# Kernel tuning notes

Measured on AMD Instinct MI355X. Metric: run time of the kernel, lower is better.

Reference implementation:

```python
import jax, jax.numpy as jnp
import numpy as np

DIM = 1024
HEADS = 16
DHEAD = 64
INNER = HEADS * DHEAD
EPS = 1e-5


def layer_norm(x, g, b):
    mu = jnp.mean(x, axis=-1, keepdims=True)
    var = jnp.mean(jnp.square(x - mu), axis=-1, keepdims=True)
    return (x - mu) * jax.lax.rsqrt(var + EPS) * g + b


def apply_rope(x, cos, sin):
    # x: [b, h, s, d]; cos/sin broadcast as [1, 1, s, d/2]
    d2 = x.shape[-1] // 2
    x1, x2 = x[..., :d2], x[..., d2:]
    return jnp.concatenate([x1 * cos - x2 * sin, x2 * cos + x1 * sin], axis=-1)


def setup_inputs() -> dict:
    key = jax.random.key(0)
    ks = jax.random.split(key, 10)
    B, N, S = 8, 256, 4096
    latents = jax.random.normal(ks[0], (B, N, DIM), dtype=jnp.float32)
    context = jax.random.normal(ks[1], (B, S, DIM), dtype=jnp.float32)
    cos = jax.random.uniform(ks[2], (S, DHEAD // 2), dtype=jnp.float32)
    sin = jax.random.uniform(ks[3], (S, DHEAD // 2), dtype=jnp.float32)
    init = lambda k, shp, fan_in: jax.random.normal(k, shp, dtype=jnp.float32) / np.sqrt(fan_in)
    return {
        "latents": latents,
        "context": context,
        "cos": cos,
        "sin": sin,
        "ln_lat_g": jnp.ones((DIM,), jnp.float32),
        "ln_lat_b": jnp.zeros((DIM,), jnp.float32),
        "ln_ctx_g": jnp.ones((DIM,), jnp.float32),
        "ln_ctx_b": jnp.zeros((DIM,), jnp.float32),
        "Wq": init(ks[4], (DIM, INNER), DIM),
        "Wkv": init(ks[5], (DIM, 2 * INNER), DIM),
        "Wo": init(ks[6], (INNER, DIM), INNER),
        "bo": jnp.zeros((DIM,), jnp.float32),
    }


def reference(latents, context, cos, sin, ln_lat_g, ln_lat_b, ln_ctx_g, ln_ctx_b, Wq, Wkv, Wo, bo):
    b, n, _ = latents.shape
    s = context.shape[1]
    lat = layer_norm(latents, ln_lat_g, ln_lat_b)
    ctx = layer_norm(context, ln_ctx_g, ln_ctx_b)
    q = (lat @ Wq).reshape(b, n, HEADS, DHEAD).transpose(0, 2, 1, 3)   # [b,h,n,d]
    kv = ctx @ Wkv
    k, v = jnp.split(kv, 2, axis=-1)
    k = k.reshape(b, s, HEADS, DHEAD).transpose(0, 2, 1, 3)           # [b,h,s,d]
    v = v.reshape(b, s, HEADS, DHEAD).transpose(0, 2, 1, 3)
    k = apply_rope(k, cos[None, None], sin[None, None])
    scale = DHEAD ** (-0.5)
    attn = jnp.einsum('bhnd,bhsd->bhns', q, k) * scale
    attn = jnp.clip(attn, -11.0, 11.0)
    attn = jax.nn.softmax(attn, axis=-1)
    out = jnp.einsum('bhns,bhsd->bhnd', attn, v)
    out = out.transpose(0, 2, 1, 3).reshape(b, n, INNER)
    return out @ Wo + bo
```

## Files before the change

kernel.cpp:

```cpp
#include <hip/hip_runtime.h>
#include <hip/hip_bf16.h>
#include <math.h>

#define DIM   1024
#define HEADS 16
#define DHEAD 64
#define NB    8
#define NLAT  256
#define SCTX  4096

typedef short bf16x8 __attribute__((ext_vector_type(8)));
typedef float f32x4  __attribute__((ext_vector_type(4)));

__device__ __forceinline__ unsigned short f2b(float f) {
    union { float f; unsigned u; } x; x.f = f;
    unsigned r = x.u + 0x7FFFu + ((x.u >> 16) & 1u);
    return (unsigned short)(r >> 16);
}

__device__ __forceinline__ unsigned pkbf16(float a, float b) {
    float2 f2; f2.x = a; f2.y = b;
    __hip_bfloat162 h = __float22bfloat162_rn(f2);
    union { __hip_bfloat162 h; unsigned u; } cv; cv.h = h;
    return cv.u;
}

#define LN_BLOCKS (NB * NLAT + NB * SCTX)
__global__ __launch_bounds__(256) void prep_all(
    const float* __restrict__ latents, const float* __restrict__ context,
    const float* __restrict__ g_lat, const float* __restrict__ b_lat,
    const float* __restrict__ g_ctx, const float* __restrict__ b_ctx,
    const float* __restrict__ Wq, const float* __restrict__ Wkv,
    const float* __restrict__ Wo,
    unsigned short* __restrict__ lat_b, unsigned short* __restrict__ ctx_b,
    unsigned short* __restrict__ Wqb, unsigned short* __restrict__ Wkvb,
    unsigned short* __restrict__ Wob)
{
    __shared__ unsigned short tile[32][33];
    int gb = blockIdx.x, t = threadIdx.x;
    if (gb < LN_BLOCKS) {
        const float* x; const float* g; const float* b; unsigned short* y; int r;
        if (gb < NB * NLAT) { x = latents; g = g_lat; b = b_lat; y = lat_b; r = gb; }
        else { x = context; g = g_ctx; b = b_ctx; y = ctx_b; r = gb - NB * NLAT; }
        float* ls = (float*)tile;
        float* lq = ls + 4;
        float* st = ls + 8;
        float4 v = ((const float4*)(x + (size_t)r * DIM))[t];
        float s  = v.x + v.y + v.z + v.w;
        float sq = v.x * v.x + v.y * v.y + v.z * v.z + v.w * v.w;
        #pragma unroll
        for (int off = 32; off > 0; off >>= 1) {
            s  += __shfl_down(s, off);
            sq += __shfl_down(sq, off);
        }
        int wid = t >> 6, lane = t & 63;
        if (lane == 0) { ls[wid] = s; lq[wid] = sq; }
        __syncthreads();
        if (t == 0) {
            s  = ls[0] + ls[1] + ls[2] + ls[3];
            sq = lq[0] + lq[1] + lq[2] + lq[3];
            float m   = s * (1.0f / DIM);
            float var = sq * (1.0f / DIM) - m * m;
            st[0] = m;
            st[1] = rsqrtf(var + 1e-5f);
        }
        __syncthreads();
        float mu = st[0], rs = st[1];
        float4 gg = ((const float4*)g)[t];
        float4 bb = ((const float4*)b)[t];
        ushort4 o;
        o.x = f2b((v.x - mu) * rs * gg.x + bb.x);
        o.y = f2b((v.y - mu) * rs * gg.y + bb.y);
        o.z = f2b((v.z - mu) * rs * gg.z + bb.z);
        o.w = f2b((v.w - mu) * rs * gg.w + bb.w);
        ((ushort4*)(y + (size_t)r * DIM))[t] = o;
    } else {
        int id = gb - LN_BLOCKS;
        int z = id >> 10, y = (id >> 5) & 31, xb = id & 31;
        const float* W; unsigned short* Wt; int N, coloff = 0;
        switch (z) {
            case 0: W = Wq;  Wt = Wqb;  N = DIM;     break;
            case 1: W = Wkv; Wt = Wkvb; N = 2 * DIM; break;
            case 2: W = Wkv; Wt = Wkvb; N = 2 * DIM; coloff = DIM; break;
            default: W = Wo; Wt = Wob;  N = DIM;     break;
        }
        int n0 = xb * 32 + coloff, k0 = y * 32;
        int tx = t & 31, ty = t >> 5;
        #pragma unroll
        for (int i = 0; i < 4; ++i) {
            int k = k0 + ty + i * 8;
            tile[tx][ty + i * 8] = f2b(W[(size_t)k * N + n0 + tx]);
        }
        __syncthreads();
        #pragma unroll
        for (int i = 0; i < 4; ++i) {
            int n = n0 + ty + i * 8;
            Wt[(size_t)n * DIM + k0 + tx] = tile[ty + i * 8][tx];
        }
    }
}

#define GK 1024

#define MFMA_Q(i0, j0)                                                         \
    _Pragma("unroll")                                                          \
    for (int ii = 0; ii < 4; ++ii) {                                           \
        _Pragma("unroll")                                                      \
        for (int jj = 0; jj < 2; ++jj) {                                       \
            acc[(i0) + ii][(j0) + jj] = __builtin_amdgcn_mfma_f32_16x16x32_bf16( \
                a[ii][0], b[(j0) + jj][0], acc[(i0) + ii][(j0) + jj], 0, 0, 0);  \
            acc[(i0) + ii][(j0) + jj] = __builtin_amdgcn_mfma_f32_16x16x32_bf16( \
                a[ii][1], b[(j0) + jj][1], acc[(i0) + ii][(j0) + jj], 0, 0, 0);  \
        }                                                                      \
    }

__global__ __launch_bounds__(512, 2) void gemm256(
    const unsigned short* __restrict__ Akv, const unsigned short* __restrict__ Bkv,
    const unsigned short* __restrict__ Aq,  const unsigned short* __restrict__ Bq,
    const float* __restrict__ cosp, const float* __restrict__ sinp,
    unsigned short* __restrict__ outk, unsigned short* __restrict__ outv,
    unsigned short* __restrict__ outq)
{
    __shared__ __align__(16) unsigned short As[2][16384];
    __shared__ __align__(16) unsigned short Bs[2][16384];

    int t = threadIdx.x;
    int w = t >> 6, l = t & 63;
    int wr = w >> 2, wc = w & 3;
    int quad = l >> 4, ln = l & 15;

    int g = blockIdx.x;
    const unsigned short* A; const unsigned short* B;
    int m_tile, n_tile, isq;
    if (g < 1024) {
        int xcd = g & 7, j = g >> 3;
        n_tile = j & 7;
        m_tile = xcd * 16 + (j >> 3);
        A = Akv; B = Bkv; isq = 0;
    } else {
        g -= 1024;
        n_tile = g & 3;
        m_tile = g >> 2;
        A = Aq; B = Bq; isq = 1;
    }
    int m_base = m_tile * 256, n_base = n_tile * 256;
    const unsigned short* Ag = A + (size_t)m_base * GK;
    const unsigned short* Bg = B + (size_t)n_base * GK;

    f32x4 acc[8][4];
    {
        f32x4 zero = {0.f, 0.f, 0.f, 0.f};
        #pragma unroll
        for (int i = 0; i < 8; ++i)
            #pragma unroll
            for (int j = 0; j < 4; ++j) acc[i][j] = zero;
    }

    int srow = l >> 3;
    int schk = ((l & 7) ^ srow) * 8;

    auto STAGE = [&](const unsigned short* src, int k0, unsigned short* dst) {
        #pragma unroll
        for (int jj = 0; jj < 2; ++jj) {
            int row = jj * 64 + w * 8 + srow;
            __builtin_amdgcn_global_load_lds(
                (const __attribute__((address_space(1))) void*)(src + (size_t)row * GK + k0 + schk),
                (__attribute__((address_space(3))) void*)(dst + row * 64 + (l & 7) * 8),
                16, 0, 0);
        }
    };

    STAGE(Ag,                     0, As[0]);
    STAGE(Ag + 128 * (size_t)GK,  0, As[0] + 8192);
    STAGE(Bg,                     0, Bs[0]);
    STAGE(Bg + 128 * (size_t)GK,  0, Bs[0] + 8192);
    STAGE(Bg,                    64, Bs[1]);
    STAGE(Bg + 128 * (size_t)GK, 64, Bs[1] + 8192);
    asm volatile("s_waitcnt vmcnt(4)" ::: "memory");
    __builtin_amdgcn_s_barrier();

    for (int kt = 0; kt < 16; ++kt) {
        int buf = kt & 1;
        const unsigned short* Ab = As[buf] + wr * 8192;
        const unsigned short* Bb = Bs[buf] + (wc >> 1) * 8192;
        int bloc = (wc & 1) * 64;
        int xs = ln & 7;
        bf16x8 a[4][2], b[4][2];

        #pragma unroll
        for (int i = 0; i < 4; ++i)
            #pragma unroll
            for (int kk = 0; kk < 2; ++kk)
                a[i][kk] = *(const bf16x8*)(Ab + (i * 16 + ln) * 64 + (((kk * 4 + quad) ^ xs) << 3));
        #pragma unroll
        for (int j = 0; j < 2; ++j)
            #pragma unroll
            for (int kk = 0; kk < 2; ++kk)
                b[j][kk] = *(const bf16x8*)(Bb + (bloc + j * 16 + ln) * 64 + (((kk * 4 + quad) ^ xs) << 3));
        if (kt + 1 < 16) {
            int k0 = (kt + 1) * 64;
            STAGE(Ag,                    k0, As[buf ^ 1]);
            STAGE(Ag + 128 * (size_t)GK, k0, As[buf ^ 1] + 8192);
        }
        __builtin_amdgcn_s_barrier();
        asm volatile("s_waitcnt lgkmcnt(0)" ::: "memory");
        __builtin_amdgcn_sched_barrier(0);
        __builtin_amdgcn_s_setprio(1);
        MFMA_Q(0, 0)
        __builtin_amdgcn_s_setprio(0);
        __builtin_amdgcn_s_barrier();

        #pragma unroll
        for (int j = 0; j < 2; ++j)
            #pragma unroll
            for (int kk = 0; kk < 2; ++kk)
                b[2 + j][kk] = *(const bf16x8*)(Bb + (bloc + (2 + j) * 16 + ln) * 64 + (((kk * 4 + quad) ^ xs) << 3));
        __builtin_amdgcn_s_barrier();
        asm volatile("s_waitcnt lgkmcnt(0)" ::: "memory");
        __builtin_amdgcn_sched_barrier(0);
        __builtin_amdgcn_s_setprio(1);
        MFMA_Q(0, 2)
        __builtin_amdgcn_s_setprio(0);
        __builtin_amdgcn_s_barrier();

        #pragma unroll
        for (int i = 0; i < 4; ++i)
            #pragma unroll
            for (int kk = 0; kk < 2; ++kk)
                a[i][kk] = *(const bf16x8*)(Ab + ((4 + i) * 16 + ln) * 64 + (((kk * 4 + quad) ^ xs) << 3));
        if (kt + 2 < 16) STAGE(Bg, (kt + 2) * 64, Bs[buf]);
        __builtin_amdgcn_s_barrier();
        asm volatile("s_waitcnt lgkmcnt(0)" ::: "memory");
        __builtin_amdgcn_sched_barrier(0);
        __builtin_amdgcn_s_setprio(1);
        MFMA_Q(4, 2)
        __builtin_amdgcn_s_setprio(0);
        __builtin_amdgcn_s_barrier();

        if (kt + 2 < 16) STAGE(Bg + 128 * (size_t)GK, (kt + 2) * 64, Bs[buf] + 8192);
        __builtin_amdgcn_s_barrier();
        __builtin_amdgcn_s_setprio(1);
        MFMA_Q(4, 0)
        __builtin_amdgcn_s_setprio(0);
        if (kt + 2 < 16) asm volatile("s_waitcnt vmcnt(4)" ::: "memory");
        else             asm volatile("s_waitcnt vmcnt(0)" ::: "memory");
        __builtin_amdgcn_s_barrier();
    }

    if (!isq) {
        if (n_base >= DIM) {
            #pragma unroll
            for (int i = 0; i < 8; ++i) {
                int s0 = m_base + wr * 128 + i * 16 + quad * 4;
                int bb = s0 >> 12, s = s0 & 4095;
                #pragma unroll
                for (int j = 0; j < 4; ++j) {
                    int n2 = n_base + wc * 64 + j * 16 + ln - DIM;
                    int h = n2 >> 6, d = n2 & 63;
                    ushort4 pk;
                    pk.x = f2b(acc[i][j][0]); pk.y = f2b(acc[i][j][1]);
                    pk.z = f2b(acc[i][j][2]); pk.w = f2b(acc[i][j][3]);
                    *(ushort4*)(outv + (((size_t)(bb * HEADS + h) * DHEAD + d) * SCTX) + s) = pk;
                }
            }
        } else {
            #pragma unroll
            for (int i = 0; i < 8; ++i) {
                #pragma unroll
                for (int r = 0; r < 4; ++r) {
                    int m = m_base + wr * 128 + i * 16 + quad * 4 + r;
                    int bb = m >> 12, s = m & 4095;
                    #pragma unroll
                    for (int j = 0; j < 2; ++j) {
                        int n = n_base + wc * 64 + j * 16 + ln;
                        int h = n >> 6, d1 = n & 63;
                        float x1 = acc[i][j][r], x2 = acc[i][j + 2][r];
                        float c  = cosp[s * 32 + d1];
                        float sn = sinp[s * 32 + d1];
                        unsigned short* kr =
                            outk + (((size_t)(bb * HEADS + h) * SCTX + s) * DHEAD) + d1;
                        kr[0]  = f2b(x1 * c - x2 * sn);
                        kr[32] = f2b(x2 * c + x1 * sn);
                    }
                }
            }
        }
    } else {
        #pragma unroll
        for (int i = 0; i < 8; ++i)
            #pragma unroll
            for (int j = 0; j < 4; ++j)
                #pragma unroll
                for (int r = 0; r < 4; ++r) {
                    int m = m_base + wr * 128 + i * 16 + quad * 4 + r;
                    int n = n_base + wc * 64 + j * 16 + ln;
                    int bb = m >> 8, nn = m & 255;
                    int h = n >> 6, d = n & 63;
                    outq[(((size_t)(bb * HEADS + h) * NLAT + nn) * DHEAD) + d] =
                        f2b(acc[i][j][r] * 0.125f);
                }
    }
}

__global__ __launch_bounds__(256, 2) void gemm_mfma(
    const unsigned short* __restrict__ A, const unsigned short* __restrict__ Bn,
    const unsigned short* __restrict__ Aq, const unsigned short* __restrict__ Bq,
    int K, const float* __restrict__ bias,
    const float* __restrict__ cosp, const float* __restrict__ sinp,
    float* __restrict__ outf,
    unsigned short* __restrict__ outk, unsigned short* __restrict__ outv,
    unsigned short* __restrict__ outq,
    int mode, int ldc)
{
    __shared__ __align__(16) unsigned short As[128 * 64];
    __shared__ __align__(16) unsigned short Bs[128 * 64];
    int t = threadIdx.x;
    int wave = t >> 6, lane = t & 63;
    int g = blockIdx.x;
    int m_tile, n_tile;
    n_tile = g & 7; m_tile = g >> 3;
    int m_base = m_tile * 128, n_base = n_tile * 128;
    int wr = wave >> 1, wc = wave & 1;
    int quad = lane >> 4, ln = lane & 15;

    f32x4 zero = {0.f, 0.f, 0.f, 0.f};
    f32x4 acc[4][4];
    #pragma unroll
    for (int i = 0; i < 4; ++i)
        #pragma unroll
        for (int j = 0; j < 4; ++j) acc[i][j] = zero;

    const unsigned short* Ag = A  + (size_t)m_base * K;
    const unsigned short* Bg = Bn + (size_t)n_base * K;

    int srow  = lane >> 3;
    int schk  = ((lane & 7) ^ srow) * 8;

    for (int k0 = 0; k0 < K; k0 += 64) {
        __syncthreads();
        #pragma unroll
        for (int j = 0; j < 4; ++j) {
            int grp = j * 4 + wave;
            int row = grp * 8 + srow;
            __builtin_amdgcn_global_load_lds(
                (const __attribute__((address_space(1))) void*)(Ag + (size_t)row * K + k0 + schk),
                (__attribute__((address_space(3))) void*)(As + grp * 512 + lane * 8),
                16, 0, 0);
            __builtin_amdgcn_global_load_lds(
                (const __attribute__((address_space(1))) void*)(Bg + (size_t)row * K + k0 + schk),
                (__attribute__((address_space(3))) void*)(Bs + grp * 512 + lane * 8),
                16, 0, 0);
        }
        __syncthreads();
        #pragma unroll
        for (int kk = 0; kk < 2; ++kk) {
            bf16x8 af[4], bfr[4];
            int slot = ((kk * 4 + quad) ^ (ln & 7)) * 8;
            #pragma unroll
            for (int i = 0; i < 4; ++i) {
                af[i]  = *(const bf16x8*)(As + (wr * 64 + i * 16 + ln) * 64 + slot);
                bfr[i] = *(const bf16x8*)(Bs + (wc * 64 + i * 16 + ln) * 64 + slot);
            }
            #pragma unroll
            for (int i = 0; i < 4; ++i)
                #pragma unroll
                for (int j = 0; j < 4; ++j)
                    acc[i][j] = __builtin_amdgcn_mfma_f32_16x16x32_bf16(af[i], bfr[j], acc[i][j], 0, 0, 0);
        }
    }

    int cl = ln, rq = quad;
    #pragma unroll
    for (int i = 0; i < 4; ++i) {
        #pragma unroll
        for (int j = 0; j < 4; ++j) {
            #pragma unroll
            for (int r = 0; r < 4; ++r) {
                int m = m_base + wr * 64 + i * 16 + rq * 4 + r;
                int n = n_base + wc * 64 + j * 16 + cl;
                outf[(size_t)m * ldc + n] = acc[i][j][r] + bias[n];
            }
        }
    }
}

__global__ __launch_bounds__(256, 2) void attn_mfma(
    const unsigned short* __restrict__ qb,
    const unsigned short* __restrict__ kb,
    const unsigned short* __restrict__ vtb,
    float* __restrict__ accp,
    float* __restrict__ lp)
{
    __shared__ __align__(16) unsigned short Ks[2][64 * 64];
    __shared__ __align__(16) unsigned short Vs[2][64 * 64];
    __shared__ __align__(16) unsigned short Ps[4 * 32 * 72];

    int t = threadIdx.x, w = t >> 6, l = t & 63;
    int bh = blockIdx.x >> 3;
    int qh = (blockIdx.x >> 2) & 1;
    int sh = blockIdx.x & 3;
    int quad = l >> 4, ln = l & 15;
    int q0 = qh * 128 + w * 32;

    bf16x8 qf[2][2];
    const unsigned short* qbase = qb + ((size_t)bh * NLAT + q0) * DHEAD;
    #pragma unroll
    for (int qsub = 0; qsub < 2; ++qsub)
        #pragma unroll
        for (int kc = 0; kc < 2; ++kc)
            qf[qsub][kc] = *(const bf16x8*)(qbase + (qsub * 16 + ln) * DHEAD + kc * 32 + quad * 8);

    f32x4 acc[2][4];
    #pragma unroll
    for (int i = 0; i < 2; ++i)
        #pragma unroll
        for (int j = 0; j < 4; ++j) acc[i][j] = (f32x4){0.f, 0.f, 0.f, 0.f};
    float lacc[2] = {0.f, 0.f};

    int srow = t >> 3;
    int schk = t & 7;
    int cpos = schk ^ (srow & 7);
    const unsigned short* kgb = kb  + (size_t)bh * SCTX * DHEAD;
    const unsigned short* vgb = vtb + (size_t)bh * DHEAD * SCTX;
    unsigned short* Pw = Ps + w * 32 * 72;

    const int s_begin = sh * 1024;
    const int NT = 1024 / 64;

    uint4 kreg[2], vreg[2];
    #pragma unroll
    for (int i = 0; i < 2; ++i) {
        int row = srow + 32 * i;
        kreg[i] = *(const uint4*)(kgb + (size_t)(s_begin + row) * DHEAD + schk * 8);
        vreg[i] = *(const uint4*)(vgb + (size_t)row * SCTX + s_begin + schk * 8);
    }
    #pragma unroll
    for (int i = 0; i < 2; ++i) {
        int row = srow + 32 * i;
        *(uint4*)(&Ks[0][row * 64 + cpos * 8]) = kreg[i];
        *(uint4*)(&Vs[0][row * 64 + cpos * 8]) = vreg[i];
    }

    for (int it = 0; it < NT; ++it) {
        int buf = it & 1;
        if (it + 1 < NT) {
            int s0n = s_begin + (it + 1) * 64;
            #pragma unroll
            for (int i = 0; i < 2; ++i) {
                int row = srow + 32 * i;
                kreg[i] = *(const uint4*)(kgb + (size_t)(s0n + row) * DHEAD + schk * 8);
                vreg[i] = *(const uint4*)(vgb + (size_t)row * SCTX + s0n + schk * 8);
            }
        }
        __syncthreads();

        #pragma unroll
        for (int msub = 0; msub < 4; ++msub) {
            bf16x8 af[2];
            #pragma unroll
            for (int kc = 0; kc < 2; ++kc) {
                int sr = msub * 16 + ln;
                int ck = (4 * kc + quad) ^ (ln & 7);
                af[kc] = *(const bf16x8*)(&Ks[buf][sr * 64 + ck * 8]);
            }
            #pragma unroll
            for (int nsub = 0; nsub < 2; ++nsub) {
                f32x4 c = {0.f, 0.f, 0.f, 0.f};
                c = __builtin_amdgcn_mfma_f32_16x16x32_bf16(af[0], qf[nsub][0], c, 0, 0, 0);
                c = __builtin_amdgcn_mfma_f32_16x16x32_bf16(af[1], qf[nsub][1], c, 0, 0, 0);
                float p[4];
                #pragma unroll
                for (int r = 0; r < 4; ++r) {
                    float sc = fminf(fmaxf(c[r], -11.f), 11.f);
                    p[r] = __expf(sc - 11.f);
                    lacc[nsub] += p[r];
                }
                uint2 pk;
                pk.x = pkbf16(p[0], p[1]);
                pk.y = pkbf16(p[2], p[3]);
                *(uint2*)(Pw + (nsub * 16 + ln) * 72 + msub * 16 + quad * 4) = pk;
            }
        }
        #pragma unroll
        for (int kc = 0; kc < 2; ++kc) {
            bf16x8 pa[2];
            #pragma unroll
            for (int qsub = 0; qsub < 2; ++qsub)
                pa[qsub] = *(const bf16x8*)(Pw + (qsub * 16 + ln) * 72 + kc * 32 + quad * 8);
            #pragma unroll
            for (int dsub = 0; dsub < 4; ++dsub) {
                int dr = dsub * 16 + ln;
                int ck = (4 * kc + quad) ^ (ln & 7);
                bf16x8 vb = *(const bf16x8*)(&Vs[buf][dr * 64 + ck * 8]);
                acc[0][dsub] = __builtin_amdgcn_mfma_f32_16x16x32_bf16(pa[0], vb, acc[0][dsub], 0, 0, 0);
                acc[1][dsub] = __builtin_amdgcn_mfma_f32_16x16x32_bf16(pa[1], vb, acc[1][dsub], 0, 0, 0);
            }
        }
        if (it + 1 < NT) {
            #pragma unroll
            for (int i = 0; i < 2; ++i) {
                int row = srow + 32 * i;
                *(uint4*)(&Ks[buf ^ 1][row * 64 + cpos * 8]) = kreg[i];
                *(uint4*)(&Vs[buf ^ 1][row * 64 + cpos * 8]) = vreg[i];
            }
        }
    }

    float* accs = accp + (size_t)sh * (NB * HEADS * NLAT * DHEAD);
    float* ls   = lp   + (size_t)sh * (NB * HEADS * NLAT);

    #pragma unroll
    for (int nsub = 0; nsub < 2; ++nsub) {
        float v = lacc[nsub];
        v += __shfl_xor(v, 16);
        v += __shfl_xor(v, 32);
        if (l < 16)
            ls[bh * NLAT + q0 + nsub * 16 + l] = v;
    }
    #pragma unroll
    for (int qsub = 0; qsub < 2; ++qsub)
        #pragma unroll
        for (int dsub = 0; dsub < 4; ++dsub)
            #pragma unroll
            for (int r = 0; r < 4; ++r) {
                int qg = q0 + qsub * 16 + quad * 4 + r;
                int dg = dsub * 16 + ln;
                accs[((size_t)bh * NLAT + qg) * DHEAD + dg] = acc[qsub][dsub][r];
            }
}

__global__ __launch_bounds__(256) void attn_finalize(
    const float* __restrict__ accp, const float* __restrict__ lp,
    unsigned short* __restrict__ aob)
{
    const int ACC = NB * HEADS * NLAT * DHEAD;
    const int LSZ = NB * HEADS * NLAT;
    int idx = blockIdx.x * 256 + threadIdx.x;
    int d = idx & 63;
    int rest = idx >> 6;
    int n = rest & 255, bh = rest >> 8;
    int b = bh >> 4, h = bh & 15;
    float a = accp[idx] + accp[idx + ACC] + accp[idx + 2 * ACC] + accp[idx + 3 * ACC];
    float l = lp[rest] + lp[rest + LSZ] + lp[rest + 2 * LSZ] + lp[rest + 3 * LSZ];
    aob[(((size_t)b * NLAT + n) * HEADS + h) * DHEAD + d] = f2b(a / l);
}

extern "C" void kernel_launch(void* const* d_in, const int* in_sizes, int n_in,
                              void* d_out, int out_size, void* d_ws, size_t ws_size,
                              hipStream_t stream) {
    const float* latents  = (const float*)d_in[0];
    const float* context  = (const float*)d_in[1];
    const float* cosp     = (const float*)d_in[2];
    const float* sinp     = (const float*)d_in[3];
    const float* ln_lat_g = (const float*)d_in[4];
    const float* ln_lat_b = (const float*)d_in[5];
    const float* ln_ctx_g = (const float*)d_in[6];
    const float* ln_ctx_b = (const float*)d_in[7];
    const float* Wq  = (const float*)d_in[8];
    const float* Wkv = (const float*)d_in[9];
    const float* Wo  = (const float*)d_in[10];
    const float* bo  = (const float*)d_in[11];
    float* out = (float*)d_out;

    char* base = (char*)d_ws;
    unsigned short* lat_b = (unsigned short*)(base + 0);
    unsigned short* ctx_b = (unsigned short*)(base + 4194304);
    unsigned short* Wqb   = (unsigned short*)(base + 71303168);
    unsigned short* Wkvb  = (unsigned short*)(base + 73400320);
    unsigned short* Wob   = (unsigned short*)(base + 77594624);
    unsigned short* q_b   = (unsigned short*)(base + 79691776);
    unsigned short* k_b   = (unsigned short*)(base + 83886080);
    unsigned short* vT_b  = (unsigned short*)(base + 150994944);
    float*          accp  = (float*)(base + 218103808);
    float*          lp    = (float*)(base + 251658240);
    unsigned short* aob   = (unsigned short*)(base + 252182528);

    hipLaunchKernelGGL(prep_all, dim3(LN_BLOCKS + 4096), dim3(256), 0, stream,
                       latents, context, ln_lat_g, ln_lat_b, ln_ctx_g, ln_ctx_b,
                       Wq, Wkv, Wo, lat_b, ctx_b, Wqb, Wkvb, Wob);
    hipLaunchKernelGGL(gemm256, dim3(1024 + 32), dim3(512), 0, stream,
                       ctx_b, Wkvb, lat_b, Wqb, cosp, sinp, k_b, vT_b, q_b);
    hipLaunchKernelGGL(attn_mfma, dim3(NB * HEADS * 8), dim3(256), 0, stream,
                       q_b, k_b, vT_b, accp, lp);
    hipLaunchKernelGGL(attn_finalize, dim3(NB * HEADS * NLAT * DHEAD / 256), dim3(256), 0, stream,
                       accp, lp, aob);
    hipLaunchKernelGGL(gemm_mfma, dim3(128), dim3(256), 0, stream,
                       aob, Wob, (const unsigned short*)nullptr, (const unsigned short*)nullptr,
                       DIM, bo,
                       (const float*)nullptr, (const float*)nullptr,
                       out, (unsigned short*)nullptr, (unsigned short*)nullptr,
                       (unsigned short*)nullptr, 0, DIM);
}
```

Baseline: 536.2 us.

## Software-pipeline LDS fragment reads against MFMA in projection GEMM

Restructures the 256x256 GEMM main loop so LDS fragment reads for the next quadrant (and the next k-tile's A and low B fragments) are issued before or during the current MFMA block, instead of waiting on lgkmcnt(0) before each block. The explicit waits and one barrier per phase are dropped, the B fragments are split into low and high halves, and the vmcnt thresholds are adjusted to the new load ordering. The goal is to hide LDS latency behind matrix math. The cost is more live registers, and correctness now depends on the compiler inserting the right waits for the cross-phase LDS reads.

```diff
diff --git a/kernel.cpp b/kernel.cpp
--- a/kernel.cpp
+++ b/kernel.cpp
@@ -102,18 +102,6 @@
 
 #define GK 1024
 
-#define MFMA_Q(i0, j0)                                                         \
-    _Pragma("unroll")                                                          \
-    for (int ii = 0; ii < 4; ++ii) {                                           \
-        _Pragma("unroll")                                                      \
-        for (int jj = 0; jj < 2; ++jj) {                                       \
-            acc[(i0) + ii][(j0) + jj] = __builtin_amdgcn_mfma_f32_16x16x32_bf16( \
-                a[ii][0], b[(j0) + jj][0], acc[(i0) + ii][(j0) + jj], 0, 0, 0);  \
-            acc[(i0) + ii][(j0) + jj] = __builtin_amdgcn_mfma_f32_16x16x32_bf16( \
-                a[ii][1], b[(j0) + jj][1], acc[(i0) + ii][(j0) + jj], 0, 0, 0);  \
-        }                                                                      \
-    }
-
 __global__ __launch_bounds__(512, 2) void gemm256(
     const unsigned short* __restrict__ Akv, const unsigned short* __restrict__ Bkv,
     const unsigned short* __restrict__ Aq,  const unsigned short* __restrict__ Bq,
@@ -158,6 +146,11 @@
 
     int srow = l >> 3;
     int schk = ((l & 7) ^ srow) * 8;
+    int bloc = (wc & 1) * 64;
+    int xs = ln & 7;
+    int koff[2];
+    koff[0] = ((quad) ^ xs) << 3;
+    koff[1] = ((4 + quad) ^ xs) << 3;
 
     auto STAGE = [&](const unsigned short* src, int k0, unsigned short* dst) {
         #pragma unroll
@@ -169,6 +162,44 @@
                 16, 0, 0);
         }
     };
+
+    bf16x8 a[4][2], bl[2][2], bh[2][2];
+
+    auto RD_A = [&](const unsigned short* base, int rowoff) {
+        #pragma unroll
+        for (int kk = 0; kk < 2; ++kk)
+            #pragma unroll
+            for (int i = 0; i < 4; ++i)
+                a[i][kk] = *(const bf16x8*)(base + (rowoff + i * 16 + ln) * 64 + koff[kk]);
+    };
+    auto RD_BL = [&](const unsigned short* base) {
+        #pragma unroll
+        for (int kk = 0; kk < 2; ++kk)
+            #pragma unroll
+            for (int j = 0; j < 2; ++j)
+                bl[j][kk] = *(const bf16x8*)(base + (bloc + j * 16 + ln) * 64 + koff[kk]);
+    };
+    auto RD_BH = [&](const unsigned short* base) {
+        #pragma unroll
+        for (int kk = 0; kk < 2; ++kk)
+            #pragma unroll
+            for (int j = 0; j < 2; ++j)
+                bh[j][kk] = *(const bf16x8*)(base + (bloc + 32 + j * 16 + ln) * 64 + koff[kk]);
+    };
+
+#define MM(i0, bb, j0)                                                          \
+    _Pragma("unroll")                                                           \
+    for (int kk = 0; kk < 2; ++kk) {                                            \
+        _Pragma("unroll")                                                       \
+        for (int ii = 0; ii < 4; ++ii) {                                        \
+            _Pragma("unroll")                                                   \
+            for (int jj = 0; jj < 2; ++jj) {                                    \
+                acc[(i0) + ii][(j0) + jj] =                                     \
+                    __builtin_amdgcn_mfma_f32_16x16x32_bf16(                    \
+                        a[ii][kk], bb[jj][kk], acc[(i0) + ii][(j0) + jj], 0, 0, 0); \
+            }                                                                   \
+        }                                                                       \
+    }
 
     STAGE(Ag,                     0, As[0]);
     STAGE(Ag + 128 * (size_t)GK,  0, As[0] + 8192);
@@ -178,74 +209,55 @@
     STAGE(Bg + 128 * (size_t)GK, 64, Bs[1] + 8192);
     asm volatile("s_waitcnt vmcnt(4)" ::: "memory");
     __builtin_amdgcn_s_barrier();
+    __builtin_amdgcn_sched_barrier(0);
+    RD_A(As[0] + wr * 8192, 0);
+    RD_BL(Bs[0] + (wc >> 1) * 8192);
 
     for (int kt = 0; kt < 16; ++kt) {
-        int buf = kt & 1;
-        const unsigned short* Ab = As[buf] + wr * 8192;
-        const unsigned short* Bb = Bs[buf] + (wc >> 1) * 8192;
-        int bloc = (wc & 1) * 64;
-        int xs = ln & 7;
-        bf16x8 a[4][2], b[4][2];
-
-        #pragma unroll
-        for (int i = 0; i < 4; ++i)
-            #pragma unroll
-            for (int kk = 0; kk < 2; ++kk)
-                a[i][kk] = *(const bf16x8*)(Ab + (i * 16 + ln) * 64 + (((kk * 4 + quad) ^ xs) << 3));
-        #pragma unroll
-        for (int j = 0; j < 2; ++j)
-            #pragma unroll
-            for (int kk = 0; kk < 2; ++kk)
-                b[j][kk] = *(const bf16x8*)(Bb + (bloc + j * 16 + ln) * 64 + (((kk * 4 + quad) ^ xs) << 3));
+        int buf = kt & 1, o = buf ^ 1;
+        const unsigned short* Ab  = As[buf] + wr * 8192;
+        const unsigned short* Abn = As[o]   + wr * 8192;
+        const unsigned short* Bb  = Bs[buf] + (wc >> 1) * 8192;
+        const unsigned short* Bbn = Bs[o]   + (wc >> 1) * 8192;
+
         if (kt + 1 < 16) {
             int k0 = (kt + 1) * 64;
-            STAGE(Ag,                    k0, As[buf ^ 1]);
-            STAGE(Ag + 128 * (size_t)GK, k0, As[buf ^ 1] + 8192);
-        }
-        __builtin_amdgcn_s_barrier();
-        asm volatile("s_waitcnt lgkmcnt(0)" ::: "memory");
-        __builtin_amdgcn_sched_barrier(0);
+            STAGE(Ag,                    k0, As[o]);
+            STAGE(Ag + 128 * (size_t)GK, k0, As[o] + 8192);
+        }
+        RD_BH(Bb);
         __builtin_amdgcn_s_setprio(1);
-        MFMA_Q(0, 0)
+        MM(0, bl, 0)
         __builtin_amdgcn_s_setprio(0);
         __builtin_amdgcn_s_barrier();
-
-        #pragma unroll
-        for (int j = 0; j < 2; ++j)
-            #pragma unroll
-            for (int kk = 0; kk < 2; ++kk)
-                b[2 + j][kk] = *(const bf16x8*)(Bb + (bloc + (2 + j) * 16 + ln) * 64 + (((kk * 4 + quad) ^ xs) << 3));
+        __builtin_amdgcn_sched_barrier(0);
+
+        __builtin_amdgcn_s_setprio(1);
+        MM(0, bh, 2)
+        __builtin_amdgcn_s_setprio(0);
+        RD_A(Ab, 64);
         __builtin_amdgcn_s_barrier();
-        asm volatile("s_waitcnt lgkmcnt(0)" ::: "memory");
         __builtin_amdgcn_sched_barrier(0);
+
+        if (kt + 2 < 16) STAGE(Bg, (kt + 2) * 64, Bs[buf]);
         __builtin_amdgcn_s_setprio(1);
-        MFMA_Q(0, 2)
+        MM(4, bl, 0)
         __builtin_amdgcn_s_setprio(0);
+        if (kt + 2 < 16)      asm volatile("s_waitcnt vmcnt(2)" ::: "memory");
+        else if (kt + 1 < 16) asm volatile("s_waitcnt vmcnt(0)" ::: "memory");
         __builtin_amdgcn_s_barrier();
-
-        #pragma unroll
-        for (int i = 0; i < 4; ++i)
-            #pragma unroll
-            for (int kk = 0; kk < 2; ++kk)
-                a[i][kk] = *(const bf16x8*)(Ab + ((4 + i) * 16 + ln) * 64 + (((kk * 4 + quad) ^ xs) << 3));
-        if (kt + 2 < 16) STAGE(Bg, (kt + 2) * 64, Bs[buf]);
+        __builtin_amdgcn_sched_barrier(0);
+
+        if (kt + 2 < 16) STAGE(Bg + 128 * (size_t)GK, (kt + 2) * 64, Bs[buf] + 8192);
+        if (kt + 1 < 16) RD_BL(Bbn);
+        __builtin_amdgcn_s_setprio(1);
+        MM(4, bh, 2)
+        __builtin_amdgcn_s_setprio(0);
+        if (kt + 1 < 16) RD_A(Abn, 0);
         __builtin_amdgcn_s_barrier();
-        asm volatile("s_waitcnt lgkmcnt(0)" ::: "memory");
         __builtin_amdgcn_sched_barrier(0);
-        __builtin_amdgcn_s_setprio(1);
-        MFMA_Q(4, 2)
-        __builtin_amdgcn_s_setprio(0);
-        __builtin_amdgcn_s_barrier();
-
-        if (kt + 2 < 16) STAGE(Bg + 128 * (size_t)GK, (kt + 2) * 64, Bs[buf] + 8192);
-        __builtin_amdgcn_s_barrier();
-        __builtin_amdgcn_s_setprio(1);
-        MFMA_Q(4, 0)
-        __builtin_amdgcn_s_setprio(0);
-        if (kt + 2 < 16) asm volatile("s_waitcnt vmcnt(4)" ::: "memory");
-        else             asm volatile("s_waitcnt vmcnt(0)" ::: "memory");
-        __builtin_amdgcn_s_barrier();
-    }
+    }
+#undef MM
 
     if (!isq) {
         if (n_base >= DIM) {
```

New measurement: 535.1 us. About the same (-0.2%).
